# Kernel tuning notes

Measured on AMD Instinct MI355X. Metric: run time of the kernel, lower is better.

Reference implementation:

```python
import jax, jax.numpy as jnp
import numpy as np

B, S, D = 128, 8192, 64  # batch, source_length, bin_rep_size (32 * 2 directions)

def setup_inputs() -> dict:
    key = jax.random.key(0)
    kx, kv = jax.random.split(key)
    x = jax.random.normal(kx, (B, S, D), dtype=jnp.float32)
    # original uses tf.random.uniform((bin_rep_size, 1))
    v = jax.random.uniform(kv, (D, 1), dtype=jnp.float32)
    return {"x": x, "v": v}

def reference(x, v):
    # scores: batched matvec against the context vector -> [B, S]
    scores = jnp.einsum('bsd,dk->bs', x, v)
    # softmax over source_length (axis=1 in original)
    alpha = jax.nn.softmax(scores, axis=1)          # [B, S]
    alpha = alpha[:, None, :]                        # [B, 1, S]
    out = jnp.matmul(alpha, x)                       # [B, 1, D]
    return (out, alpha)
```

## Files before the change

kernel.cpp:

```cpp
#include <hip/hip_runtime.h>
#include <math.h>

#define BB 128
#define SS 8192
#define DD 64
#define KP 8
#define ROWS_PER_BLOCK (SS / KP)
#define THREADS 256

__global__ __launch_bounds__(THREADS) void k1_partial(
    const float* __restrict__ x, const float* __restrict__ v,
    float* __restrict__ alpha_out,
    float* __restrict__ acc_p,
    float* __restrict__ l_p)
{
    const int blk  = blockIdx.x;
    const int b    = blk / KP;
    const int p    = blk % KP;
    const int tid  = threadIdx.x;
    const int wave = tid >> 6;
    const int lane = tid & 63;
    const int q    = lane & 15;
    const int r    = lane >> 4;

    const float4 v4 = ((const float4*)v)[q];

    const int rows_per_wave = ROWS_PER_BLOCK / 4;
    const int iters         = rows_per_wave / 4;
    const int s_base        = p * ROWS_PER_BLOCK + wave * rows_per_wave;
    const float* xb = x + (size_t)b * SS * DD;

    float4 acc = make_float4(0.f, 0.f, 0.f, 0.f);
    float lsum = 0.f;

    #pragma unroll 4
    for (int i = 0; i < iters; ++i) {
        const int srow = s_base + i * 4;
        const float4 x4 = ((const float4*)(xb + (size_t)srow * DD))[lane];

        float sc = x4.x * v4.x + x4.y * v4.y + x4.z * v4.z + x4.w * v4.w;
        sc += __shfl_xor(sc, 1);
        sc += __shfl_xor(sc, 2);
        sc += __shfl_xor(sc, 4);
        sc += __shfl_xor(sc, 8);

        const float w = __expf(sc);
        if (q == 0) {
            alpha_out[(size_t)b * SS + srow + r] = w;
            lsum += w;
        }
        acc.x += w * x4.x;
        acc.y += w * x4.y;
        acc.z += w * x4.z;
        acc.w += w * x4.w;
    }

    acc.x += __shfl_xor(acc.x, 16); acc.x += __shfl_xor(acc.x, 32);
    acc.y += __shfl_xor(acc.y, 16); acc.y += __shfl_xor(acc.y, 32);
    acc.z += __shfl_xor(acc.z, 16); acc.z += __shfl_xor(acc.z, 32);
    acc.w += __shfl_xor(acc.w, 16); acc.w += __shfl_xor(acc.w, 32);
    lsum  += __shfl_xor(lsum, 16);  lsum  += __shfl_xor(lsum, 32);

    __shared__ float s_acc[4][DD];
    __shared__ float s_l[4];
    if (r == 0) {
        ((float4*)s_acc[wave])[q] = acc;
        if (q == 0) s_l[wave] = lsum;
    }
    __syncthreads();

    if (tid < DD) {
        const float a = s_acc[0][tid] + s_acc[1][tid] + s_acc[2][tid] + s_acc[3][tid];
        acc_p[((size_t)b * KP + p) * DD + tid] = a;
    }
    if (tid == 0) {
        l_p[b * KP + p] = s_l[0] + s_l[1] + s_l[2] + s_l[3];
    }
}

__global__ __launch_bounds__(DD) void k2_combine(
    const float* __restrict__ acc_p, const float* __restrict__ l_p,
    float* __restrict__ out, float* __restrict__ inv_l)
{
    const int b = blockIdx.x;
    const int d = threadIdx.x;
    float a = 0.f;
    #pragma unroll
    for (int p = 0; p < KP; ++p) a += acc_p[((size_t)b * KP + p) * DD + d];
    float l = 0.f;
    #pragma unroll
    for (int p = 0; p < KP; ++p) l += l_p[b * KP + p];
    const float il = 1.0f / l;
    out[b * DD + d] = a * il;
    if (d == 0) inv_l[b] = il;
}

__global__ __launch_bounds__(256) void k3_scale(
    float* __restrict__ alpha, const float* __restrict__ inv_l)
{
    const int idx = blockIdx.x * 256 + threadIdx.x;
    const int b = idx >> 13;
    alpha[idx] *= inv_l[b];
}

extern "C" void kernel_launch(void* const* d_in, const int* in_sizes, int n_in,
                              void* d_out, int out_size, void* d_ws, size_t ws_size,
                              hipStream_t stream) {
    const float* x = (const float*)d_in[0];
    const float* v = (const float*)d_in[1];

    float* out   = (float*)d_out;
    float* alpha = (float*)d_out + BB * DD;

    float* acc_p = (float*)d_ws;
    float* l_p   = acc_p + BB * KP * DD;
    float* inv_l = l_p + BB * KP;

    k1_partial<<<BB * KP, THREADS, 0, stream>>>(x, v, alpha, acc_p, l_p);
    k2_combine<<<BB, DD, 0, stream>>>(acc_p, l_p, out, inv_l);
    k3_scale<<<(BB * SS) / 256, 256, 0, stream>>>(alpha, inv_l);
}
```

Measured before the change: 362.6 us.

## Batch x loads ahead of compute, use DPP row reductions, double block threads

The main loop now issues eight independent float4 loads before any dependent math, giving more memory-level parallelism per wave. The 16-lane dot-product reduction uses DPP row operations instead of ds_swizzle/bpermute shuffles. The block grows to 512 threads (8 waves), with the shared-memory combine generalised to match. The cost is higher register use per thread, which may reduce occupancy.

```diff
diff --git a/kernel.cpp b/kernel.cpp
--- a/kernel.cpp
+++ b/kernel.cpp
@@ -6,7 +6,22 @@
 #define DD 64
 #define KP 8
 #define ROWS_PER_BLOCK (SS / KP)
-#define THREADS 256
+#define THREADS 512
+#define NWAVES (THREADS / 64)
+#define UNROLL 8
+
+__device__ __forceinline__ float row_sum16(float x) {
+    int t;
+    t = __builtin_amdgcn_update_dpp(0, __float_as_int(x), 0xB1, 0xF, 0xF, true);
+    x += __int_as_float(t);
+    t = __builtin_amdgcn_update_dpp(0, __float_as_int(x), 0x4E, 0xF, 0xF, true);
+    x += __int_as_float(t);
+    t = __builtin_amdgcn_update_dpp(0, __float_as_int(x), 0x141, 0xF, 0xF, true);
+    x += __int_as_float(t);
+    t = __builtin_amdgcn_update_dpp(0, __float_as_int(x), 0x140, 0xF, 0xF, true);
+    x += __int_as_float(t);
+    return x;
+}
 
 __global__ __launch_bounds__(THREADS) void k1_partial(
     const float* __restrict__ x, const float* __restrict__ v,
@@ -25,7 +40,7 @@
 
     const float4 v4 = ((const float4*)v)[q];
 
-    const int rows_per_wave = ROWS_PER_BLOCK / 4;
+    const int rows_per_wave = ROWS_PER_BLOCK / NWAVES;
     const int iters         = rows_per_wave / 4;
     const int s_base        = p * ROWS_PER_BLOCK + wave * rows_per_wave;
     const float* xb = x + (size_t)b * SS * DD;
@@ -33,26 +48,29 @@
     float4 acc = make_float4(0.f, 0.f, 0.f, 0.f);
     float lsum = 0.f;
 
-    #pragma unroll 4
-    for (int i = 0; i < iters; ++i) {
-        const int srow = s_base + i * 4;
-        const float4 x4 = ((const float4*)(xb + (size_t)srow * DD))[lane];
-
-        float sc = x4.x * v4.x + x4.y * v4.y + x4.z * v4.z + x4.w * v4.w;
-        sc += __shfl_xor(sc, 1);
-        sc += __shfl_xor(sc, 2);
-        sc += __shfl_xor(sc, 4);
-        sc += __shfl_xor(sc, 8);
-
-        const float w = __expf(sc);
-        if (q == 0) {
-            alpha_out[(size_t)b * SS + srow + r] = w;
-            lsum += w;
+    for (int i0 = 0; i0 < iters; i0 += UNROLL) {
+        float4 xs[UNROLL];
+        #pragma unroll
+        for (int u = 0; u < UNROLL; ++u) {
+            const int srow = s_base + (i0 + u) * 4;
+            xs[u] = ((const float4*)(xb + (size_t)srow * DD))[lane];
         }
-        acc.x += w * x4.x;
-        acc.y += w * x4.y;
-        acc.z += w * x4.z;
-        acc.w += w * x4.w;
+        #pragma unroll
+        for (int u = 0; u < UNROLL; ++u) {
+            const int srow = s_base + (i0 + u) * 4;
+            const float4 x4 = xs[u];
+            float sc = x4.x * v4.x + x4.y * v4.y + x4.z * v4.z + x4.w * v4.w;
+            sc = row_sum16(sc);
+            const float w = __expf(sc);
+            if (q == 0) {
+                alpha_out[(size_t)b * SS + srow + r] = w;
+                lsum += w;
+            }
+            acc.x += w * x4.x;
+            acc.y += w * x4.y;
+            acc.z += w * x4.z;
+            acc.w += w * x4.w;
+        }
     }
 
     acc.x += __shfl_xor(acc.x, 16); acc.x += __shfl_xor(acc.x, 32);
@@ -61,8 +79,8 @@
     acc.w += __shfl_xor(acc.w, 16); acc.w += __shfl_xor(acc.w, 32);
     lsum  += __shfl_xor(lsum, 16);  lsum  += __shfl_xor(lsum, 32);
 
-    __shared__ float s_acc[4][DD];
-    __shared__ float s_l[4];
+    __shared__ float s_acc[NWAVES][DD];
+    __shared__ float s_l[NWAVES];
     if (r == 0) {
         ((float4*)s_acc[wave])[q] = acc;
         if (q == 0) s_l[wave] = lsum;
@@ -70,11 +88,16 @@
     __syncthreads();
 
     if (tid < DD) {
-        const float a = s_acc[0][tid] + s_acc[1][tid] + s_acc[2][tid] + s_acc[3][tid];
+        float a = 0.f;
+        #pragma unroll
+        for (int w = 0; w < NWAVES; ++w) a += s_acc[w][tid];
         acc_p[((size_t)b * KP + p) * DD + tid] = a;
     }
     if (tid == 0) {
-        l_p[b * KP + p] = s_l[0] + s_l[1] + s_l[2] + s_l[3];
+        float l = 0.f;
+        #pragma unroll
+        for (int w = 0; w < NWAVES; ++w) l += s_l[w];
+        l_p[b * KP + p] = l;
     }
 }
 
```

New measurement: 352.6 us. -2.8%, faster.
